# Kernel tuning notes

Measured on AMD Instinct MI355X. Metric: run time of the kernel, lower is better.

## Reference

```python
import jax, jax.numpy as jnp
import numpy as np

N_NODES = 100000
N_EDGES = 3200000
HIDDEN = 64
OUT = 30


def _graph_conv(x, src, dst, W, b, n_nodes):
    # DGL GraphConv with norm='both': D_out^{-1/2} -> aggregate -> D_in^{-1/2} -> W -> +b
    ones = jnp.ones(src.shape[0], dtype=x.dtype)
    deg_out = jax.ops.segment_sum(ones, src, num_segments=n_nodes)
    deg_in = jax.ops.segment_sum(ones, dst, num_segments=n_nodes)
    norm_out = jnp.where(deg_out > 0, jax.lax.rsqrt(jnp.maximum(deg_out, 1e-30)), 0.0)
    norm_in = jnp.where(deg_in > 0, jax.lax.rsqrt(jnp.maximum(deg_in, 1e-30)), 0.0)
    h = x * norm_out[:, None]                    # [N, F] scaled source features
    msg = h[src]                                 # [E, F] gather
    agg = jax.ops.segment_sum(msg, dst, num_segments=n_nodes)  # [N, F] scatter-add
    agg = agg * norm_in[:, None]
    return agg @ W + b


def setup_inputs() -> dict:
    key = jax.random.key(0)
    k1, k2, k3, k4, k5 = jax.random.split(key, 5)
    x = jax.random.normal(k1, (N_NODES, HIDDEN), dtype=jnp.float32)
    src = jax.random.randint(k2, (N_EDGES,), 0, N_NODES, dtype=jnp.int32)
    dst = jax.random.randint(k3, (N_EDGES,), 0, N_NODES, dtype=jnp.int32)
    W1 = jax.random.normal(k4, (HIDDEN, HIDDEN), dtype=jnp.float32) / np.sqrt(HIDDEN)
    b1 = jnp.zeros((HIDDEN,), dtype=jnp.float32)
    W2 = jax.random.normal(k5, (HIDDEN, OUT), dtype=jnp.float32) / np.sqrt(HIDDEN)
    b2 = jnp.zeros((OUT,), dtype=jnp.float32)
    return {"x": x, "src": src, "dst": dst, "W1": W1, "b1": b1, "W2": W2, "b2": b2}


def reference(x, src, dst, W1, b1, W2, b2):
    h = _graph_conv(x, src, dst, W1, b1, N_NODES)
    h = jax.nn.relu(h)                           # conv1 activation=F.relu
    out = _graph_conv(h, src, dst, W2, b2, N_NODES)  # conv2: no activation
    return out
```

## Files before the change

kernel.cpp:

```cpp
#include <hip/hip_runtime.h>


#define NN 100000
#define NE 3200000
#define NOUTF 30
#define TPB 256
#define TPBW 1024
#define TPBS 1024

#define DSH 7
#define DCB 128
#define DNB ((NN + DCB - 1) / DCB)
#define SSH 8
#define SCB 256
#define SNB ((NN + SCB - 1) / SCB)

#define CHUNK 8192
#define NBLK ((NE + CHUNK - 1) / CHUNK)
#define HLD (DNB * NBLK)
#define HLS (SNB * NBLK)
#define HLT (HLD + HLS)

#define GCH 1024
#define NSC ((HLT + GCH - 1) / GCH)

#define POOL 4608

__device__ __forceinline__ unsigned short f2bf(float f) {
  unsigned u = __float_as_uint(f);
  u = (u + 0x7FFFu + ((u >> 16) & 1u)) >> 16;
  return (unsigned short)u;
}

__device__ __forceinline__ void acc8(float* a, const uint4& u) {
  a[0] += __uint_as_float(u.x << 16);
  a[1] += __uint_as_float(u.x & 0xFFFF0000u);
  a[2] += __uint_as_float(u.y << 16);
  a[3] += __uint_as_float(u.y & 0xFFFF0000u);
  a[4] += __uint_as_float(u.z << 16);
  a[5] += __uint_as_float(u.z & 0xFFFF0000u);
  a[6] += __uint_as_float(u.w << 16);
  a[7] += __uint_as_float(u.w & 0xFFFF0000u);
}

__device__ __forceinline__ int xcd_swz(int orig, int n) {
  int q = n / 8, r = n % 8;
  int xcd = orig % 8, idx = orig / 8;
  return (xcd < r ? xcd * (q + 1) : r * (q + 1) + (xcd - r) * q) + idx;
}

__global__ __launch_bounds__(TPBW) void k_hist(const int* __restrict__ src,
                                               const int* __restrict__ dst,
                                               int* __restrict__ H) {
  __shared__ int hd[DNB], hs[SNB];
  int t = threadIdx.x, k = blockIdx.x;
  for (int b = t; b < DNB; b += TPBW) hd[b] = 0;
  for (int b = t; b < SNB; b += TPBW) hs[b] = 0;
  __syncthreads();
  int beg = k * CHUNK, end = min(NE, beg + CHUNK);
  for (int i = beg + t; i < end; i += TPBW) {
    atomicAdd(&hd[dst[i] >> DSH], 1);
    atomicAdd(&hs[src[i] >> SSH], 1);
  }
  __syncthreads();
  for (int b = t; b < DNB; b += TPBW) H[b * NBLK + k] = hd[b];
  for (int b = t; b < SNB; b += TPBW) H[HLD + b * NBLK + k] = hs[b];
}

__global__ __launch_bounds__(TPB) void g_scan1(const int* __restrict__ a,
                                               int* __restrict__ bsums) {
  int t = threadIdx.x;
  int base = blockIdx.x * GCH + t * 4;
  int s = 0;
#pragma unroll
  for (int j = 0; j < 4; ++j) { int idx = base + j; if (idx < HLT) s += a[idx]; }
  __shared__ int red[TPB];
  red[t] = s; __syncthreads();
  for (int off = TPB / 2; off > 0; off >>= 1) {
    if (t < off) red[t] += red[t + off];
    __syncthreads();
  }
  if (t == 0) bsums[blockIdx.x] = red[0];
}

__global__ __launch_bounds__(TPB) void g_scan3(int* __restrict__ a,
                                               const int* __restrict__ bsums) {
  __shared__ int lds[TPB];
  __shared__ int sc[512];
  int t = threadIdx.x;
  {
    int i0 = 2 * t, i1 = 2 * t + 1;
    int v0 = (i0 < NSC) ? bsums[i0] : 0;
    int v1 = (i1 < NSC) ? bsums[i1] : 0;
    int s2 = v0 + v1;
    int acc = s2; lds[t] = acc; __syncthreads();
    for (int off = 1; off < TPB; off <<= 1) {
      int add = (t >= off) ? lds[t - off] : 0; __syncthreads();
      acc += add; lds[t] = acc; __syncthreads();
    }
    int excl = acc - s2;
    sc[i0] = excl;
    sc[i1] = excl + v0;
  }
  __syncthreads();
  int pref = sc[blockIdx.x];
  __syncthreads();
  int base = blockIdx.x * GCH + t * 4;
  int v[4]; int s = 0;
#pragma unroll
  for (int j = 0; j < 4; ++j) {
    int idx = base + j;
    v[j] = (idx < HLT) ? a[idx] : 0;
    s += v[j];
  }
  int acc = s; lds[t] = acc; __syncthreads();
  for (int off = 1; off < TPB; off <<= 1) {
    int add = (t >= off) ? lds[t - off] : 0; __syncthreads();
    acc += add; lds[t] = acc; __syncthreads();
  }
  int run = pref + (acc - s);
#pragma unroll
  for (int j = 0; j < 4; ++j) {
    int idx = base + j;
    if (idx < HLT) a[idx] = run;
    run += v[j];
  }
}

__global__ __launch_bounds__(TPBS) void k_scatter(const int* __restrict__ src,
                                                  const int* __restrict__ dst,
                                                  const int* __restrict__ Hsc,
                                                  int* __restrict__ packed,
                                                  unsigned char* __restrict__ ss) {
  __shared__ unsigned short perm_d[CHUNK];
  __shared__ unsigned short perm_s[CHUNK];
  __shared__ int curD[DNB], adjD[DNB];
  __shared__ int curS[SNB], adjS[SNB];
  __shared__ int scanbuf[TPBS];
  int t = threadIdx.x;
  int k = xcd_swz((int)blockIdx.x, NBLK);
  int beg = k * CHUNK, end = min(NE, beg + CHUNK);
  int cnt = end - beg;

  {
    int st = 0, c = 0;
    if (t < DNB) {
      int idx = t * NBLK + k;
      st = Hsc[idx];
      int en = (idx + 1 < HLT) ? Hsc[idx + 1] : 2 * NE;
      c = en - st;
    }
    int acc = c; scanbuf[t] = acc; __syncthreads();
    for (int off = 1; off < TPBS; off <<= 1) {
      int add = (t >= off) ? scanbuf[t - off] : 0; __syncthreads();
      acc += add; scanbuf[t] = acc; __syncthreads();
    }
    int excl = acc - c;
    if (t < DNB) { curD[t] = excl; adjD[t] = st - excl; }
  }
  __syncthreads();
  {
    int st = 0, c = 0;
    if (t < SNB) {
      int idx = HLD + t * NBLK + k;
      st = Hsc[idx];
      int en = (idx + 1 < HLT) ? Hsc[idx + 1] : 2 * NE;
      c = en - st;
    }
    int acc = c; scanbuf[t] = acc; __syncthreads();
    for (int off = 1; off < TPBS; off <<= 1) {
      int add = (t >= off) ? scanbuf[t - off] : 0; __syncthreads();
      acc += add; scanbuf[t] = acc; __syncthreads();
    }
    int excl = acc - c;
    if (t < SNB) { curS[t] = excl; adjS[t] = (st - NE) - excl; }
  }
  __syncthreads();

  for (int i = beg + t; i < end; i += TPBS) {
    int s = src[i], d = dst[i];
    int li = i - beg;
    int p = atomicAdd(&curD[d >> DSH], 1);
    perm_d[p] = (unsigned short)li;
    int q = atomicAdd(&curS[s >> SSH], 1);
    perm_s[q] = (unsigned short)li;
  }
  __syncthreads();

  for (int i = t; i < cnt; i += TPBS) {
    int gi = beg + perm_d[i];
    int d = dst[gi], s = src[gi];
    packed[adjD[d >> DSH] + i] = (s << DSH) | (d & (DCB - 1));
  }
  for (int i = t; i < cnt; i += TPBS) {
    int s = src[beg + perm_s[i]];
    ss[adjS[s >> SSH] + i] = (unsigned char)(s & (SCB - 1));
  }
}

__global__ __launch_bounds__(TPB) void k_fine(const int* __restrict__ Hsc,
                                              const int* __restrict__ packed,
                                              const unsigned char* __restrict__ ss,
                                              int* __restrict__ src_sorted,
                                              int* __restrict__ row_ptr,
                                              float* __restrict__ norm_in,
                                              float* __restrict__ norm_out) {
  __shared__ int hist[DCB], scn[DCB], cur[DCB];
  __shared__ int pool[POOL];
  __shared__ int histS[SCB];
  int t = threadIdx.x;
  if (blockIdx.x < DNB) {
    int b = blockIdx.x;
    int seg_beg = Hsc[b * NBLK];
    int seg_end = (b + 1 < DNB) ? Hsc[(b + 1) * NBLK] : NE;
    int cnt = seg_end - seg_beg;
    if (t < DCB) hist[t] = 0;
    __syncthreads();
    for (int i = seg_beg + t; i < seg_end; i += TPB)
      atomicAdd(&hist[packed[i] & (DCB - 1)], 1);
    __syncthreads();
    if (t < DCB) scn[t] = hist[t];
    __syncthreads();
    for (int off = 1; off < DCB; off <<= 1) {
      int add = (t >= off && t < DCB) ? scn[t - off] : 0;
      __syncthreads();
      if (t < DCB) scn[t] += add;
      __syncthreads();
    }
    if (t < DCB) {
      int excl = scn[t] - hist[t];
      cur[t] = excl;
      int node = b * DCB + t;
      if (node < NN) {
        row_ptr[node] = seg_beg + excl;
        norm_in[node] = (hist[t] > 0) ? rsqrtf((float)hist[t]) : 0.0f;
      }
    }
    if (b == DNB - 1 && t == 0) row_ptr[NN] = NE;
    __syncthreads();
    for (int i = seg_beg + t; i < seg_end; i += TPB) {
      int v = packed[i];
      int p = atomicAdd(&cur[v & (DCB - 1)], 1);
      int sv = v >> DSH;
      if (p < POOL) pool[p] = sv;
      else src_sorted[seg_beg + p] = sv;
    }
    __syncthreads();
    int lim = min(cnt, POOL);
    for (int i = t; i < lim; i += TPB) src_sorted[seg_beg + i] = pool[i];
  } else {
    int b = blockIdx.x - DNB;
    int seg_beg = Hsc[HLD + b * NBLK] - NE;
    int seg_end = (b + 1 < SNB) ? Hsc[HLD + (b + 1) * NBLK] - NE : NE;
    if (t < SCB) histS[t] = 0;
    __syncthreads();
    for (int i = seg_beg + t; i < seg_end; i += TPB)
      atomicAdd(&histS[ss[i]], 1);
    __syncthreads();
    if (t < SCB) {
      int node = b * SCB + t;
      if (node < NN)
        norm_out[node] = (histS[t] > 0) ? rsqrtf((float)histS[t]) : 0.0f;
    }
  }
}

__global__ __launch_bounds__(TPB) void k_gemm1(const float4* __restrict__ x4,
                                               const float* __restrict__ W1,
                                               const float* __restrict__ norm_out,
                                               unsigned short* __restrict__ xt_b) {
  int lane = threadIdx.x & 63;
  int wid = (blockIdx.x * TPB + threadIdx.x) >> 6;
  int nwaves = gridDim.x * (TPB / 64);
  float w[64];
#pragma unroll
  for (int k = 0; k < 64; ++k) w[k] = W1[k * 64 + lane];
  int m = lane >> 4, q = lane & 15;
  for (int grp = wid; grp < NN / 4; grp += nwaves) {
    int nbase = grp * 4;
    float4 rv = x4[(nbase + m) * 16 + q];
    int r0 = __float_as_int(rv.x), r1 = __float_as_int(rv.y);
    int r2 = __float_as_int(rv.z), r3 = __float_as_int(rv.w);
    float acc[4] = {0.f, 0.f, 0.f, 0.f};
#pragma unroll
    for (int mm = 0; mm < 4; ++mm) {
#pragma unroll
      for (int ql = 0; ql < 16; ++ql) {
        int sl = mm * 16 + ql;
        acc[mm] = fmaf(__int_as_float(__builtin_amdgcn_readlane(r0, sl)), w[ql * 4 + 0], acc[mm]);
        acc[mm] = fmaf(__int_as_float(__builtin_amdgcn_readlane(r1, sl)), w[ql * 4 + 1], acc[mm]);
        acc[mm] = fmaf(__int_as_float(__builtin_amdgcn_readlane(r2, sl)), w[ql * 4 + 2], acc[mm]);
        acc[mm] = fmaf(__int_as_float(__builtin_amdgcn_readlane(r3, sl)), w[ql * 4 + 3], acc[mm]);
      }
    }
#pragma unroll
    for (int mm = 0; mm < 4; ++mm) {
      int n = nbase + mm;
      xt_b[n * 64 + lane] = f2bf(norm_out[n] * acc[mm]);
    }
  }
}

__global__ __launch_bounds__(TPB) void k_agg1(const uint4* __restrict__ xt4,
                                              const int* __restrict__ src_sorted,
                                              const int* __restrict__ row_ptr,
                                              const float* __restrict__ norm_in,
                                              const float* __restrict__ b1,
                                              uint4* __restrict__ h1_b4) {
  int node = (blockIdx.x * TPB + threadIdx.x) >> 6;
  int lane = threadIdx.x & 63;
  int slot = lane >> 3;
  int fl = lane & 7;
  int beg = row_ptr[node];
  int end = row_ptr[node + 1];
  float a[8] = {0.f, 0.f, 0.f, 0.f, 0.f, 0.f, 0.f, 0.f};
  int e = beg + slot;
  for (; e + 8 < end; e += 16) {
    int s0 = src_sorted[e];
    int s1 = src_sorted[e + 8];
    uint4 u0 = xt4[s0 * 8 + fl];
    uint4 u1 = xt4[s1 * 8 + fl];
    acc8(a, u0);
    acc8(a, u1);
  }
  if (e < end) {
    uint4 u0 = xt4[src_sorted[e] * 8 + fl];
    acc8(a, u0);
  }
#pragma unroll
  for (int off = 8; off <= 32; off <<= 1) {
#pragma unroll
    for (int j = 0; j < 8; ++j) a[j] += __shfl_xor(a[j], off);
  }
  if (slot == 0) {
    float ni = norm_in[node];
    const float4* b1_4 = reinterpret_cast<const float4*>(b1);
    float4 bl = b1_4[fl * 2];
    float4 bh = b1_4[fl * 2 + 1];
    float v0 = fmaxf(fmaf(a[0], ni, bl.x), 0.f);
    float v1 = fmaxf(fmaf(a[1], ni, bl.y), 0.f);
    float v2 = fmaxf(fmaf(a[2], ni, bl.z), 0.f);
    float v3 = fmaxf(fmaf(a[3], ni, bl.w), 0.f);
    float v4 = fmaxf(fmaf(a[4], ni, bh.x), 0.f);
    float v5 = fmaxf(fmaf(a[5], ni, bh.y), 0.f);
    float v6 = fmaxf(fmaf(a[6], ni, bh.z), 0.f);
    float v7 = fmaxf(fmaf(a[7], ni, bh.w), 0.f);
    uint4 o;
    o.x = (unsigned)f2bf(v0) | ((unsigned)f2bf(v1) << 16);
    o.y = (unsigned)f2bf(v2) | ((unsigned)f2bf(v3) << 16);
    o.z = (unsigned)f2bf(v4) | ((unsigned)f2bf(v5) << 16);
    o.w = (unsigned)f2bf(v6) | ((unsigned)f2bf(v7) << 16);
    h1_b4[node * 8 + fl] = o;
  }
}

__global__ __launch_bounds__(TPB) void k_gemm2b(const uint4* __restrict__ h1b4,
                                                const float* __restrict__ W2,
                                                const float* __restrict__ norm_out,
                                                unsigned short* __restrict__ h1t_b) {
  int lane = threadIdx.x & 63;
  int wid = (blockIdx.x * TPB + threadIdx.x) >> 6;
  int nwaves = gridDim.x * (TPB / 64);
  int oc = lane & 31;
  float w[64];
#pragma unroll
  for (int k = 0; k < 64; ++k)
    w[k] = (oc < NOUTF) ? W2[k * NOUTF + oc] : 0.f;
  int r = lane >> 3, q = lane & 7;
  for (int grp = wid; grp < NN / 8; grp += nwaves) {
    int nbase = grp * 8;
    uint4 rv = h1b4[(nbase + r) * 8 + q];
    int v0 = (int)rv.x, v1 = (int)rv.y, v2 = (int)rv.z, v3 = (int)rv.w;
#pragma unroll
    for (int rr = 0; rr < 8; ++rr) {
      float acc0 = 0.f, acc1 = 0.f;
#pragma unroll
      for (int qq = 0; qq < 8; ++qq) {
        int sl = rr * 8 + qq;
        unsigned u0 = (unsigned)__builtin_amdgcn_readlane(v0, sl);
        unsigned u1 = (unsigned)__builtin_amdgcn_readlane(v1, sl);
        unsigned u2 = (unsigned)__builtin_amdgcn_readlane(v2, sl);
        unsigned u3 = (unsigned)__builtin_amdgcn_readlane(v3, sl);
        acc0 = fmaf(__uint_as_float(u0 << 16),          w[qq * 8 + 0], acc0);
        acc1 = fmaf(__uint_as_float(u0 & 0xFFFF0000u), w[qq * 8 + 1], acc1);
        acc0 = fmaf(__uint_as_float(u1 << 16),          w[qq * 8 + 2], acc0);
        acc1 = fmaf(__uint_as_float(u1 & 0xFFFF0000u), w[qq * 8 + 3], acc1);
        acc0 = fmaf(__uint_as_float(u2 << 16),          w[qq * 8 + 4], acc0);
        acc1 = fmaf(__uint_as_float(u2 & 0xFFFF0000u), w[qq * 8 + 5], acc1);
        acc0 = fmaf(__uint_as_float(u3 << 16),          w[qq * 8 + 6], acc0);
        acc1 = fmaf(__uint_as_float(u3 & 0xFFFF0000u), w[qq * 8 + 7], acc1);
      }
      int n = nbase + rr;
      if (lane < 32) {
        float acc = acc0 + acc1;
        unsigned short hv = (oc < NOUTF) ? f2bf(norm_out[n] * acc) : (unsigned short)0;
        h1t_b[n * 32 + oc] = hv;
      }
    }
  }
}

__global__ __launch_bounds__(TPB) void k_agg2(const uint4* __restrict__ h1t4,
                                              const int* __restrict__ src_sorted,
                                              const int* __restrict__ row_ptr,
                                              const float* __restrict__ norm_in,
                                              const float* __restrict__ b2,
                                              float* __restrict__ out) {
  int node = (blockIdx.x * TPB + threadIdx.x) >> 6;
  int lane = threadIdx.x & 63;
  int slot = lane >> 2;
  int fl = lane & 3;
  int beg = row_ptr[node];
  int end = row_ptr[node + 1];
  float a[8] = {0.f, 0.f, 0.f, 0.f, 0.f, 0.f, 0.f, 0.f};
  int e = beg + slot;
  for (; e + 16 < end; e += 32) {
    int s0 = src_sorted[e];
    int s1 = src_sorted[e + 16];
    uint4 u0 = h1t4[s0 * 4 + fl];
    uint4 u1 = h1t4[s1 * 4 + fl];
    acc8(a, u0);
    acc8(a, u1);
  }
  if (e < end) {
    uint4 u0 = h1t4[src_sorted[e] * 4 + fl];
    acc8(a, u0);
  }
#pragma unroll
  for (int off = 4; off <= 32; off <<= 1) {
#pragma unroll
    for (int j = 0; j < 8; ++j) a[j] += __shfl_xor(a[j], off);
  }
  if (slot == 0) {
    float ni = norm_in[node];
    int f0 = fl * 8;
    float2* ob = (float2*)(out + (size_t)node * NOUTF);
#pragma unroll
    for (int p = 0; p < 4; ++p) {
      int f = f0 + p * 2;
      if (f < NOUTF) {
        float2 v;
        v.x = fmaf(a[p * 2], ni, b2[f]);
        v.y = fmaf(a[p * 2 + 1], ni, b2[f + 1]);
        ob[f >> 1] = v;
      }
    }
  }
}

extern "C" void kernel_launch(void* const* d_in, const int* in_sizes, int n_in,
                              void* d_out, int out_size, void* d_ws, size_t ws_size,
                              hipStream_t stream) {
  (void)in_sizes; (void)n_in; (void)out_size; (void)ws_size;
  const float* x = (const float*)d_in[0];
  const int* src = (const int*)d_in[1];
  const int* dst = (const int*)d_in[2];
  const float* W1 = (const float*)d_in[3];
  const float* b1 = (const float*)d_in[4];
  const float* W2 = (const float*)d_in[5];
  const float* b2 = (const float*)d_in[6];
  float* out = (float*)d_out;

  char* ws = (char*)d_ws;
  int* row_ptr = (int*)(ws + 0);
  float* norm_out = (float*)(ws + 400128);
  float* norm_in = (float*)(ws + 800128);
  int* H = (int*)(ws + 1200128);
  int* bsums = (int*)(ws + 3100128);
  unsigned char* ss = (unsigned char*)(ws + 3101952);
  int* src_sorted = (int*)(ws + 8365696);
  int* packed = (int*)(ws + 21165696);
  uint4* h1_b4 = (uint4*)(ws + 21165696);
  unsigned short* xt_b = (unsigned short*)(ws + 46765696);
  unsigned short* h1t_b = (unsigned short*)(ws + 46765696);

  k_hist<<<NBLK, TPBW, 0, stream>>>(src, dst, H);
  g_scan1<<<NSC, TPB, 0, stream>>>(H, bsums);
  g_scan3<<<NSC, TPB, 0, stream>>>(H, bsums);
  k_scatter<<<NBLK, TPBS, 0, stream>>>(src, dst, H, packed, ss);
  k_fine<<<DNB + SNB, TPB, 0, stream>>>(H, packed, ss, src_sorted, row_ptr, norm_in, norm_out);
  k_gemm1<<<1024, TPB, 0, stream>>>((const float4*)x, W1, norm_out, xt_b);
  k_agg1<<<NN / 4, TPB, 0, stream>>>((const uint4*)xt_b, src_sorted, row_ptr,
                                     norm_in, b1, h1_b4);
  k_gemm2b<<<1024, TPB, 0, stream>>>((const uint4*)h1_b4, W2, norm_out, h1t_b);
  k_agg2<<<NN / 4, TPB, 0, stream>>>((const uint4*)h1t_b, src_sorted, row_ptr, norm_in, b2, out);
}
```

Before: 231.7 us.

## Vectorize edge loads, use wave-shuffle scans, stage payloads in LDS during sort

The histogram and scatter kernels now load eight edges per thread with int4 vector loads. The LDS-based block scans are replaced with wavefront shuffle scans, which cuts the number of barriers. The scatter kernel now writes the packed payloads and source values into LDS directly, so it no longer re-gathers src/dst from global memory through a permutation. The fine sort caches the packed values in the shared pool on its first pass, so it reads them from global only once, but its final writes to src_sorted become scattered.

```diff
diff --git a/kernel.cpp b/kernel.cpp
--- a/kernel.cpp
+++ b/kernel.cpp
@@ -49,6 +49,33 @@
   return (xcd < r ? xcd * (q + 1) : r * (q + 1) + (xcd - r) * q) + idx;
 }
 
+template <int NT>
+__device__ __forceinline__ int blk_exscan(int val, int* wsums, int t) {
+  __syncthreads();
+  int lane = t & 63;
+  int inc = val;
+#pragma unroll
+  for (int off = 1; off < 64; off <<= 1) {
+    int n = __shfl_up(inc, off);
+    if (lane >= off) inc += n;
+  }
+  if (lane == 63) wsums[t >> 6] = inc;
+  __syncthreads();
+  constexpr int NW = NT / 64;
+  if (t < NW) {
+    int v = wsums[t];
+    int acc = v;
+#pragma unroll
+    for (int off = 1; off < NW; off <<= 1) {
+      int n = __shfl_up(acc, off);
+      if (t >= off) acc += n;
+    }
+    wsums[t] = acc - v;
+  }
+  __syncthreads();
+  return wsums[t >> 6] + inc - val;
+}
+
 __global__ __launch_bounds__(TPBW) void k_hist(const int* __restrict__ src,
                                                const int* __restrict__ dst,
                                                int* __restrict__ H) {
@@ -58,9 +85,25 @@
   for (int b = t; b < SNB; b += TPBW) hs[b] = 0;
   __syncthreads();
   int beg = k * CHUNK, end = min(NE, beg + CHUNK);
-  for (int i = beg + t; i < end; i += TPBW) {
-    atomicAdd(&hd[dst[i] >> DSH], 1);
-    atomicAdd(&hs[src[i] >> SSH], 1);
+  int cnt = end - beg;
+  int ebase = t * 8;
+  if (ebase + 8 <= cnt) {
+    const int4* s4 = (const int4*)(src + beg + ebase);
+    const int4* d4 = (const int4*)(dst + beg + ebase);
+    int4 a0 = s4[0], a1 = s4[1], b0 = d4[0], b1 = d4[1];
+    int sv[8] = {a0.x, a0.y, a0.z, a0.w, a1.x, a1.y, a1.z, a1.w};
+    int dv[8] = {b0.x, b0.y, b0.z, b0.w, b1.x, b1.y, b1.z, b1.w};
+#pragma unroll
+    for (int j = 0; j < 8; ++j) {
+      atomicAdd(&hd[dv[j] >> DSH], 1);
+      atomicAdd(&hs[sv[j] >> SSH], 1);
+    }
+  } else {
+    for (int j = 0; j < 8 && ebase + j < cnt; ++j) {
+      int i = beg + ebase + j;
+      atomicAdd(&hd[dst[i] >> DSH], 1);
+      atomicAdd(&hs[src[i] >> SSH], 1);
+    }
   }
   __syncthreads();
   for (int b = t; b < DNB; b += TPBW) H[b * NBLK + k] = hd[b];
@@ -74,37 +117,27 @@
   int s = 0;
 #pragma unroll
   for (int j = 0; j < 4; ++j) { int idx = base + j; if (idx < HLT) s += a[idx]; }
-  __shared__ int red[TPB];
-  red[t] = s; __syncthreads();
-  for (int off = TPB / 2; off > 0; off >>= 1) {
-    if (t < off) red[t] += red[t + off];
-    __syncthreads();
-  }
-  if (t == 0) bsums[blockIdx.x] = red[0];
+#pragma unroll
+  for (int off = 32; off >= 1; off >>= 1) s += __shfl_xor(s, off);
+  __shared__ int red[4];
+  if ((t & 63) == 0) red[t >> 6] = s;
+  __syncthreads();
+  if (t == 0) bsums[blockIdx.x] = red[0] + red[1] + red[2] + red[3];
 }
 
 __global__ __launch_bounds__(TPB) void g_scan3(int* __restrict__ a,
                                                const int* __restrict__ bsums) {
-  __shared__ int lds[TPB];
   __shared__ int sc[512];
+  __shared__ int wsums[4];
   int t = threadIdx.x;
-  {
-    int i0 = 2 * t, i1 = 2 * t + 1;
-    int v0 = (i0 < NSC) ? bsums[i0] : 0;
-    int v1 = (i1 < NSC) ? bsums[i1] : 0;
-    int s2 = v0 + v1;
-    int acc = s2; lds[t] = acc; __syncthreads();
-    for (int off = 1; off < TPB; off <<= 1) {
-      int add = (t >= off) ? lds[t - off] : 0; __syncthreads();
-      acc += add; lds[t] = acc; __syncthreads();
-    }
-    int excl = acc - s2;
-    sc[i0] = excl;
-    sc[i1] = excl + v0;
-  }
+  int i0 = 2 * t, i1 = 2 * t + 1;
+  int v0 = (i0 < NSC) ? bsums[i0] : 0;
+  int v1 = (i1 < NSC) ? bsums[i1] : 0;
+  int ex2 = blk_exscan<TPB>(v0 + v1, wsums, t);
+  sc[i0] = ex2;
+  sc[i1] = ex2 + v0;
   __syncthreads();
   int pref = sc[blockIdx.x];
-  __syncthreads();
   int base = blockIdx.x * GCH + t * 4;
   int v[4]; int s = 0;
 #pragma unroll
@@ -113,12 +146,8 @@
     v[j] = (idx < HLT) ? a[idx] : 0;
     s += v[j];
   }
-  int acc = s; lds[t] = acc; __syncthreads();
-  for (int off = 1; off < TPB; off <<= 1) {
-    int add = (t >= off) ? lds[t - off] : 0; __syncthreads();
-    acc += add; lds[t] = acc; __syncthreads();
-  }
-  int run = pref + (acc - s);
+  int ex = blk_exscan<TPB>(s, wsums, t);
+  int run = pref + ex;
 #pragma unroll
   for (int j = 0; j < 4; ++j) {
     int idx = base + j;
@@ -132,68 +161,69 @@
                                                   const int* __restrict__ Hsc,
                                                   int* __restrict__ packed,
                                                   unsigned char* __restrict__ ss) {
-  __shared__ unsigned short perm_d[CHUNK];
-  __shared__ unsigned short perm_s[CHUNK];
+  __shared__ int pay_lds[CHUNK];
+  __shared__ unsigned short bkt_lds[CHUNK];
+  __shared__ int s_lds[CHUNK];
   __shared__ int curD[DNB], adjD[DNB];
   __shared__ int curS[SNB], adjS[SNB];
-  __shared__ int scanbuf[TPBS];
+  __shared__ int wsums[16];
   int t = threadIdx.x;
   int k = xcd_swz((int)blockIdx.x, NBLK);
   int beg = k * CHUNK, end = min(NE, beg + CHUNK);
   int cnt = end - beg;
 
-  {
-    int st = 0, c = 0;
-    if (t < DNB) {
-      int idx = t * NBLK + k;
-      st = Hsc[idx];
-      int en = (idx + 1 < HLT) ? Hsc[idx + 1] : 2 * NE;
-      c = en - st;
-    }
-    int acc = c; scanbuf[t] = acc; __syncthreads();
-    for (int off = 1; off < TPBS; off <<= 1) {
-      int add = (t >= off) ? scanbuf[t - off] : 0; __syncthreads();
-      acc += add; scanbuf[t] = acc; __syncthreads();
-    }
-    int excl = acc - c;
-    if (t < DNB) { curD[t] = excl; adjD[t] = st - excl; }
-  }
-  __syncthreads();
-  {
-    int st = 0, c = 0;
-    if (t < SNB) {
-      int idx = HLD + t * NBLK + k;
-      st = Hsc[idx];
-      int en = (idx + 1 < HLT) ? Hsc[idx + 1] : 2 * NE;
-      c = en - st;
-    }
-    int acc = c; scanbuf[t] = acc; __syncthreads();
-    for (int off = 1; off < TPBS; off <<= 1) {
-      int add = (t >= off) ? scanbuf[t - off] : 0; __syncthreads();
-      acc += add; scanbuf[t] = acc; __syncthreads();
-    }
-    int excl = acc - c;
-    if (t < SNB) { curS[t] = excl; adjS[t] = (st - NE) - excl; }
-  }
-  __syncthreads();
-
-  for (int i = beg + t; i < end; i += TPBS) {
-    int s = src[i], d = dst[i];
-    int li = i - beg;
-    int p = atomicAdd(&curD[d >> DSH], 1);
-    perm_d[p] = (unsigned short)li;
-    int q = atomicAdd(&curS[s >> SSH], 1);
-    perm_s[q] = (unsigned short)li;
-  }
-  __syncthreads();
-
+  int stD = 0, cD = 0;
+  if (t < DNB) {
+    int idx = t * NBLK + k;
+    stD = Hsc[idx];
+    int en = (idx + 1 < HLT) ? Hsc[idx + 1] : 2 * NE;
+    cD = en - stD;
+  }
+  int exD = blk_exscan<TPBS>(cD, wsums, t);
+  if (t < DNB) { curD[t] = exD; adjD[t] = stD - exD; }
+  int stS = 0, cS = 0;
+  if (t < SNB) {
+    int idx = HLD + t * NBLK + k;
+    stS = Hsc[idx];
+    int en = (idx + 1 < HLT) ? Hsc[idx + 1] : 2 * NE;
+    cS = en - stS;
+  }
+  int exS = blk_exscan<TPBS>(cS, wsums, t);
+  if (t < SNB) { curS[t] = exS; adjS[t] = (stS - NE) - exS; }
+  __syncthreads();
+
+  int ebase = t * 8;
+  if (ebase < cnt) {
+    int sv[8], dv[8];
+    int nv;
+    if (ebase + 8 <= cnt) {
+      const int4* s4 = (const int4*)(src + beg + ebase);
+      const int4* d4 = (const int4*)(dst + beg + ebase);
+      int4 a0 = s4[0], a1 = s4[1], b0 = d4[0], b1 = d4[1];
+      sv[0] = a0.x; sv[1] = a0.y; sv[2] = a0.z; sv[3] = a0.w;
+      sv[4] = a1.x; sv[5] = a1.y; sv[6] = a1.z; sv[7] = a1.w;
+      dv[0] = b0.x; dv[1] = b0.y; dv[2] = b0.z; dv[3] = b0.w;
+      dv[4] = b1.x; dv[5] = b1.y; dv[6] = b1.z; dv[7] = b1.w;
+      nv = 8;
+    } else {
+      nv = cnt - ebase;
+      for (int j = 0; j < nv; ++j) { sv[j] = src[beg + ebase + j]; dv[j] = dst[beg + ebase + j]; }
+    }
+    for (int j = 0; j < nv; ++j) {
+      int bk = dv[j] >> DSH;
+      int p = atomicAdd(&curD[bk], 1);
+      pay_lds[p] = (sv[j] << DSH) | (dv[j] & (DCB - 1));
+      bkt_lds[p] = (unsigned short)bk;
+      int q = atomicAdd(&curS[sv[j] >> SSH], 1);
+      s_lds[q] = sv[j];
+    }
+  }
+  __syncthreads();
+
+  for (int i = t; i < cnt; i += TPBS)
+    packed[adjD[bkt_lds[i]] + i] = pay_lds[i];
   for (int i = t; i < cnt; i += TPBS) {
-    int gi = beg + perm_d[i];
-    int d = dst[gi], s = src[gi];
-    packed[adjD[d >> DSH] + i] = (s << DSH) | (d & (DCB - 1));
-  }
-  for (int i = t; i < cnt; i += TPBS) {
-    int s = src[beg + perm_s[i]];
+    int s = s_lds[i];
     ss[adjS[s >> SSH] + i] = (unsigned char)(s & (SCB - 1));
   }
 }
@@ -214,10 +244,16 @@
     int seg_beg = Hsc[b * NBLK];
     int seg_end = (b + 1 < DNB) ? Hsc[(b + 1) * NBLK] : NE;
     int cnt = seg_end - seg_beg;
+    int lim = min(cnt, POOL);
     if (t < DCB) hist[t] = 0;
     __syncthreads();
-    for (int i = seg_beg + t; i < seg_end; i += TPB)
-      atomicAdd(&hist[packed[i] & (DCB - 1)], 1);
+    for (int i = t; i < lim; i += TPB) {
+      int v = packed[seg_beg + i];
+      pool[i] = v;
+      atomicAdd(&hist[v & (DCB - 1)], 1);
+    }
+    for (int i = lim + t; i < cnt; i += TPB)
+      atomicAdd(&hist[packed[seg_beg + i] & (DCB - 1)], 1);
     __syncthreads();
     if (t < DCB) scn[t] = hist[t];
     __syncthreads();
@@ -238,16 +274,16 @@
     }
     if (b == DNB - 1 && t == 0) row_ptr[NN] = NE;
     __syncthreads();
-    for (int i = seg_beg + t; i < seg_end; i += TPB) {
-      int v = packed[i];
+    for (int i = t; i < lim; i += TPB) {
+      int v = pool[i];
       int p = atomicAdd(&cur[v & (DCB - 1)], 1);
-      int sv = v >> DSH;
-      if (p < POOL) pool[p] = sv;
-      else src_sorted[seg_beg + p] = sv;
-    }
-    __syncthreads();
-    int lim = min(cnt, POOL);
-    for (int i = t; i < lim; i += TPB) src_sorted[seg_beg + i] = pool[i];
+      src_sorted[seg_beg + p] = v >> DSH;
+    }
+    for (int i = lim + t; i < cnt; i += TPB) {
+      int v = packed[seg_beg + i];
+      int p = atomicAdd(&cur[v & (DCB - 1)], 1);
+      src_sorted[seg_beg + p] = v >> DSH;
+    }
   } else {
     int b = blockIdx.x - DNB;
     int seg_beg = Hsc[HLD + b * NBLK] - NE;
```

New measurement: 224.4 us. 3.2% less time.
